# Kernel optimization log

Hardware: AMD Instinct MI355X
Metric: run time of the kernel (lower is better)

The kernel has to match this reference:

```python
import jax, jax.numpy as jnp
import numpy as np

B, S, DIN, DOUT = 4, 512, 4096, 10240


def setup_inputs() -> dict:
    key = jax.random.key(0)
    k1, k2, k3, k4 = jax.random.split(key, 4)
    # Activation in fp16, as the module casts input to self.dtype (fp16)
    input_tensor = jax.random.normal(k1, (B, S, DIN), dtype=jnp.float32).astype(jnp.float16)
    # weight emulates fp8 e4m3 storage; values here stand in for the dequant source
    weight = jax.random.normal(k2, (DOUT, DIN), dtype=jnp.float32) * 0.02
    # per-output-channel scale, stored fp32
    weight_scale = jax.random.uniform(k3, (DOUT, 1), dtype=jnp.float32, minval=0.5, maxval=1.5)
    bias = (jax.random.normal(k4, (DOUT,), dtype=jnp.float32) * 0.02).astype(jnp.float16)
    return {"input_tensor": input_tensor, "weight": weight, "weight_scale": weight_scale, "bias": bias}


def reference(input_tensor, weight, weight_scale, bias):
    # Dequantize: fp8 weight -> fp16, multiply by per-row scale (cast to fp16)
    w16 = weight.astype(jnp.float16) * weight_scale.astype(jnp.float16)  # [DOUT, DIN]
    # F.linear: x @ W^T + b, all in fp16
    out = jnp.einsum('bsi,oi->bso', input_tensor, w16) + bias  # [B, S, DOUT]
    return out
```

## Files before the change

### kernel.cpp

```cpp
#include <hip/hip_runtime.h>
#include <hip/hip_fp16.h>

typedef _Float16 half8 __attribute__((ext_vector_type(8)));
typedef float f32x4 __attribute__((ext_vector_type(4)));

constexpr int M = 2048;
constexpr int N = 10240;
constexpr int K = 4096;

__global__ __launch_bounds__(256)
void dequant_w_kernel(const float* __restrict__ W, const float* __restrict__ Wsc,
                      _Float16* __restrict__ Wh) {
    const long total = (long)N * K / 8;
    for (long i = (long)blockIdx.x * blockDim.x + threadIdx.x; i < total;
         i += (long)gridDim.x * blockDim.x) {
        const long base = i * 8;
        const int row = (int)(base >> 12);
        const _Float16 s = (_Float16)Wsc[row];
        const float4 w0 = ((const float4*)(W + base))[0];
        const float4 w1 = ((const float4*)(W + base))[1];
        half8 h;
        h[0] = (_Float16)w0.x * s; h[1] = (_Float16)w0.y * s;
        h[2] = (_Float16)w0.z * s; h[3] = (_Float16)w0.w * s;
        h[4] = (_Float16)w1.x * s; h[5] = (_Float16)w1.y * s;
        h[6] = (_Float16)w1.z * s; h[7] = (_Float16)w1.w * s;
        *(half8*)(Wh + base) = h;
    }
}

__global__ __launch_bounds__(256)
void convert_a_kernel(const float* __restrict__ A, _Float16* __restrict__ Ah) {
    const long total = (long)M * K / 8;
    for (long i = (long)blockIdx.x * blockDim.x + threadIdx.x; i < total;
         i += (long)gridDim.x * blockDim.x) {
        const long base = i * 8;
        const float4 a0 = ((const float4*)(A + base))[0];
        const float4 a1 = ((const float4*)(A + base))[1];
        half8 h;
        h[0] = (_Float16)a0.x; h[1] = (_Float16)a0.y;
        h[2] = (_Float16)a0.z; h[3] = (_Float16)a0.w;
        h[4] = (_Float16)a1.x; h[5] = (_Float16)a1.y;
        h[6] = (_Float16)a1.z; h[7] = (_Float16)a1.w;
        *(half8*)(Ah + base) = h;
    }
}

constexpr int BM = 128, BN = 320, BK = 64;
constexpr int AELE = BM * BK;
constexpr int BELE = BN * BK;
constexpr int NT = K / BK;

#define BAR()   asm volatile("s_barrier" ::: "memory")
#define LGKM0() asm volatile("s_waitcnt lgkmcnt(0)" ::: "memory")

__device__ __forceinline__ half8 lds_rd(const _Float16* base, int row, int eo) {
    const int ps = (eo >> 3) ^ (row & 7);
    return *(const half8*)(base + row * BK + ps * 8);
}

__global__ __launch_bounds__(512, 1)
void qgemm320_kernel(const _Float16* __restrict__ Ag,
                     const _Float16* __restrict__ Wg,
                     const float*    __restrict__ bias,
                     float*          __restrict__ C)
{
    __shared__ _Float16 AsF[2 * AELE];
    __shared__ _Float16 BsF[2 * BELE];

    const int orig = blockIdx.x;
    const int wgid = (orig & 7) * 64 + (orig >> 3);
    const int m0 = (wgid & 15) * BM;
    const int n0 = (wgid >> 4) * BN;

    const int tid  = threadIdx.x;
    const int lane = tid & 63;
    const int w    = tid >> 6;
    const int wm   = w >> 2;
    const int wn   = w & 3;
    const int fr   = lane & 15;
    const int fkE  = (lane >> 4) * 8;

    const int trow  = tid >> 3;
    const int swcol = (((tid & 7) ^ (trow & 7))) * 8;

    auto stage_a = [&](int b, int u, int kcol) {
        const _Float16* src = Ag + (size_t)(m0 + u * 64 + trow) * K + (kcol + swcol);
        __builtin_amdgcn_global_load_lds(
            (const __attribute__((address_space(1))) void*)src,
            (__attribute__((address_space(3))) void*)(AsF + b * AELE + u * 4096 + tid * 8),
            16, 0, 0);
    };
    auto stage_b = [&](int b, int u, int kcol) {
        const _Float16* src = Wg + (size_t)(n0 + u * 64 + trow) * K + (kcol + swcol);
        __builtin_amdgcn_global_load_lds(
            (const __attribute__((address_space(1))) void*)src,
            (__attribute__((address_space(3))) void*)(BsF + b * BELE + u * 4096 + tid * 8),
            16, 0, 0);
    };

    f32x4 acc[4][5];
#pragma unroll
    for (int i = 0; i < 4; ++i)
#pragma unroll
        for (int j = 0; j < 5; ++j)
            acc[i][j] = (f32x4){0.f, 0.f, 0.f, 0.f};

    stage_a(0, 0, 0); stage_a(0, 1, 0);
#pragma unroll
    for (int u = 0; u < 5; ++u) stage_b(0, u, 0);
    stage_a(1, 0, BK); stage_a(1, 1, BK);
#pragma unroll
    for (int u = 0; u < 5; ++u) stage_b(1, u, BK);
    asm volatile("s_waitcnt vmcnt(7)" ::: "memory");
    BAR();

#pragma unroll 1
    for (int t = 0; t < NT; ++t) {
        const int cur = t & 1;
        const _Float16* Ab = AsF + cur * AELE;
        const _Float16* Bb = BsF + cur * BELE;
        const bool pf2 = (t + 2 < NT);
        const int k2 = (t + 2) * BK;

        half8 af[4][2], bf[5][2];

#pragma unroll
        for (int rb = 0; rb < 4; ++rb)
#pragma unroll
            for (int kh = 0; kh < 2; ++kh)
                af[rb][kh] = lds_rd(Ab, wm * 64 + rb * 16 + fr, kh * 32 + fkE);
#pragma unroll
        for (int cb = 0; cb < 5; ++cb)
#pragma unroll
            for (int kh = 0; kh < 2; ++kh)
                bf[cb][kh] = lds_rd(Bb, wn * 80 + cb * 16 + fr, kh * 32 + fkE);

        __builtin_amdgcn_s_setprio(1);
#pragma unroll
        for (int rb = 0; rb < 4; ++rb)
#pragma unroll
            for (int cb = 0; cb < 3; ++cb)
#pragma unroll
                for (int kh = 0; kh < 2; ++kh)
                    acc[rb][cb] = __builtin_amdgcn_mfma_f32_16x16x32_f16(
                        af[rb][kh], bf[cb][kh], acc[rb][cb], 0, 0, 0);
        __builtin_amdgcn_s_setprio(0);

        LGKM0();
        BAR();

        if (pf2) {
            stage_a(cur, 0, k2); stage_a(cur, 1, k2);
#pragma unroll
            for (int u = 0; u < 5; ++u) stage_b(cur, u, k2);
        }
        __builtin_amdgcn_s_setprio(1);
#pragma unroll
        for (int rb = 0; rb < 4; ++rb)
#pragma unroll
            for (int cb = 3; cb < 5; ++cb)
#pragma unroll
                for (int kh = 0; kh < 2; ++kh)
                    acc[rb][cb] = __builtin_amdgcn_mfma_f32_16x16x32_f16(
                        af[rb][kh], bf[cb][kh], acc[rb][cb], 0, 0, 0);
        __builtin_amdgcn_s_setprio(0);

        if (pf2) asm volatile("s_waitcnt vmcnt(7)" ::: "memory");
        else     asm volatile("s_waitcnt vmcnt(0)" ::: "memory");
        BAR();
    }

    float bb[5];
#pragma unroll
    for (int j = 0; j < 5; ++j)
        bb[j] = bias[n0 + wn * 80 + j * 16 + fr];
#pragma unroll
    for (int i = 0; i < 4; ++i) {
        const int row = m0 + wm * 64 + i * 16 + (lane >> 4) * 4;
#pragma unroll
        for (int j = 0; j < 5; ++j) {
            const int col = n0 + wn * 80 + j * 16 + fr;
#pragma unroll
            for (int r = 0; r < 4; ++r)
                C[(size_t)(row + r) * N + col] =
                    (float)(_Float16)(acc[i][j][r] + bb[j]);
        }
    }
}

__global__ __launch_bounds__(256, 2)
void qlinear_fused_kernel(const float* __restrict__ A, const float* __restrict__ W,
                          const float* __restrict__ Wsc, const float* __restrict__ bias,
                          float* __restrict__ C)
{
    __shared__ _Float16 As[128][64];
    __shared__ _Float16 Bs[128][64];

    const int nwg  = (M / 128) * (N / 128);
    const int orig = blockIdx.x;
    const int wgid = (orig & 7) * (nwg >> 3) + (orig >> 3);
    const int brow = wgid & (M / 128 - 1);
    const int bcol = wgid / (M / 128);
    const int m0 = brow * 128;
    const int n0 = bcol * 128;

    const int t    = threadIdx.x;
    const int lane = t & 63;
    const int wave = t >> 6;
    const int wr = (wave >> 1) * 64;
    const int wc = (wave & 1) * 64;
    const int fr = lane & 15;
    const int fk = (lane >> 4) * 8;
    const int srow = t >> 3;
    const int scol = (t & 7) * 8;

    _Float16 hs[4];
#pragma unroll
    for (int p = 0; p < 4; ++p)
        hs[p] = (_Float16)Wsc[n0 + srow + p * 32];

    f32x4 acc[4][4];
#pragma unroll
    for (int i = 0; i < 4; ++i)
#pragma unroll
        for (int j = 0; j < 4; ++j)
            acc[i][j] = (f32x4){0.f, 0.f, 0.f, 0.f};

    for (int k0 = 0; k0 < K; k0 += 64) {
        __syncthreads();
#pragma unroll
        for (int c = 0; c < 4; ++c) {
            const int rl = c * 32 + srow;
            const float* asrc = A + (size_t)(m0 + rl) * K + (k0 + scol);
            const float4 a0 = ((const float4*)asrc)[0];
            const float4 a1 = ((const float4*)asrc)[1];
            half8 av;
            av[0] = (_Float16)a0.x; av[1] = (_Float16)a0.y;
            av[2] = (_Float16)a0.z; av[3] = (_Float16)a0.w;
            av[4] = (_Float16)a1.x; av[5] = (_Float16)a1.y;
            av[6] = (_Float16)a1.z; av[7] = (_Float16)a1.w;
            *(half8*)&As[rl][scol] = av;
        }
#pragma unroll
        for (int p = 0; p < 4; ++p) {
            const int nl = srow + p * 32;
            const float* wsrc = W + (size_t)(n0 + nl) * K + (k0 + scol);
            const float4 w0 = ((const float4*)wsrc)[0];
            const float4 w1 = ((const float4*)wsrc)[1];
            half8 hv;
            hv[0] = (_Float16)w0.x * hs[p]; hv[1] = (_Float16)w0.y * hs[p];
            hv[2] = (_Float16)w0.z * hs[p]; hv[3] = (_Float16)w0.w * hs[p];
            hv[4] = (_Float16)w1.x * hs[p]; hv[5] = (_Float16)w1.y * hs[p];
            hv[6] = (_Float16)w1.z * hs[p]; hv[7] = (_Float16)w1.w * hs[p];
            *(half8*)&Bs[nl][scol] = hv;
        }
        __syncthreads();
#pragma unroll
        for (int kk = 0; kk < 64; kk += 32) {
            half8 av[4], bv[4];
#pragma unroll
            for (int i = 0; i < 4; ++i)
                av[i] = *(const half8*)&As[wr + i * 16 + fr][kk + fk];
#pragma unroll
            for (int j = 0; j < 4; ++j)
                bv[j] = *(const half8*)&Bs[wc + j * 16 + fr][kk + fk];
#pragma unroll
            for (int i = 0; i < 4; ++i)
#pragma unroll
                for (int j = 0; j < 4; ++j)
                    acc[i][j] = __builtin_amdgcn_mfma_f32_16x16x32_f16(
                        av[i], bv[j], acc[i][j], 0, 0, 0);
        }
    }
#pragma unroll
    for (int i = 0; i < 4; ++i) {
        const int row = m0 + wr + i * 16 + (lane >> 4) * 4;
#pragma unroll
        for (int j = 0; j < 4; ++j) {
            const int col = n0 + wc + j * 16 + fr;
            const float bbf = bias[col];
#pragma unroll
            for (int r = 0; r < 4; ++r)
                C[(size_t)(row + r) * N + col] =
                    (float)(_Float16)(acc[i][j][r] + bbf);
        }
    }
}

extern "C" void kernel_launch(void* const* d_in, const int* in_sizes, int n_in,
                              void* d_out, int out_size, void* d_ws, size_t ws_size,
                              hipStream_t stream) {
    const float* A    = (const float*)d_in[0];
    const float* W    = (const float*)d_in[1];
    const float* Wsc  = (const float*)d_in[2];
    const float* bias = (const float*)d_in[3];
    float* C = (float*)d_out;

    const size_t a_bytes = (size_t)M * K * sizeof(_Float16);
    const size_t w_bytes = (size_t)N * K * sizeof(_Float16);

    if (ws_size >= a_bytes + w_bytes) {
        _Float16* Ah = (_Float16*)d_ws;
        _Float16* Wh = (_Float16*)((char*)d_ws + a_bytes);
        convert_a_kernel<<<dim3(1024), dim3(256), 0, stream>>>(A, Ah);
        dequant_w_kernel<<<dim3(2048), dim3(256), 0, stream>>>(W, Wsc, Wh);
        const int nwg = (M / BM) * (N / BN);
        qgemm320_kernel<<<dim3(nwg), dim3(512), 0, stream>>>(Ah, Wh, bias, C);
    } else {
        const int nwg = (M / 128) * (N / 128);
        qlinear_fused_kernel<<<dim3(nwg), dim3(256), 0, stream>>>(A, W, Wsc, bias, C);
    }
}
```

Baseline: 231.5 us.

## Stream B fragments directly from global into registers, keep only A in LDS

The GEMM kernel no longer stages the weight tile in shared memory. Each wave loads its B fragments straight from global memory into registers, prefetching the next K-step between MFMA groups, while A still goes through a double-buffered swizzled LDS tile filled with register loads and ds writes instead of global_load_lds. This shrinks LDS use and allows two workgroups per CU (launch bounds 512,2). In exchange, B reads are uncoalesced per-lane 16-byte loads with no reuse across the four waves that share columns, and each K-step now has two barriers.

Result: slower. 374.2 us (+61.7%).

```diff
diff --git a/kernel.cpp b/kernel.cpp
--- a/kernel.cpp
+++ b/kernel.cpp
@@ -47,7 +47,6 @@
 
 constexpr int BM = 128, BN = 320, BK = 64;
 constexpr int AELE = BM * BK;
-constexpr int BELE = BN * BK;
 constexpr int NT = K / BK;
 
 #define BAR()   asm volatile("s_barrier" ::: "memory")
@@ -58,14 +57,13 @@
     return *(const half8*)(base + row * BK + ps * 8);
 }
 
-__global__ __launch_bounds__(512, 1)
-void qgemm320_kernel(const _Float16* __restrict__ Ag,
-                     const _Float16* __restrict__ Wg,
-                     const float*    __restrict__ bias,
-                     float*          __restrict__ C)
+__global__ __launch_bounds__(512, 2)
+void qgemm_bstream_kernel(const _Float16* __restrict__ Ag,
+                          const _Float16* __restrict__ Wg,
+                          const float*    __restrict__ bias,
+                          float*          __restrict__ C)
 {
     __shared__ _Float16 AsF[2 * AELE];
-    __shared__ _Float16 BsF[2 * BELE];
 
     const int orig = blockIdx.x;
     const int wgid = (orig & 7) * 64 + (orig >> 3);
@@ -80,23 +78,14 @@
     const int fr   = lane & 15;
     const int fkE  = (lane >> 4) * 8;
 
-    const int trow  = tid >> 3;
-    const int swcol = (((tid & 7) ^ (trow & 7))) * 8;
-
-    auto stage_a = [&](int b, int u, int kcol) {
-        const _Float16* src = Ag + (size_t)(m0 + u * 64 + trow) * K + (kcol + swcol);
-        __builtin_amdgcn_global_load_lds(
-            (const __attribute__((address_space(1))) void*)src,
-            (__attribute__((address_space(3))) void*)(AsF + b * AELE + u * 4096 + tid * 8),
-            16, 0, 0);
-    };
-    auto stage_b = [&](int b, int u, int kcol) {
-        const _Float16* src = Wg + (size_t)(n0 + u * 64 + trow) * K + (kcol + swcol);
-        __builtin_amdgcn_global_load_lds(
-            (const __attribute__((address_space(1))) void*)src,
-            (__attribute__((address_space(3))) void*)(BsF + b * BELE + u * 4096 + tid * 8),
-            16, 0, 0);
-    };
+    const int arow   = tid >> 2;
+    const int aslot0 = (tid & 3) * 2;
+    const int acol   = aslot0 * 8;
+
+    const _Float16* bsrc[5];
+#pragma unroll
+    for (int cb = 0; cb < 5; ++cb)
+        bsrc[cb] = Wg + (size_t)(n0 + wn * 80 + cb * 16 + fr) * K + fkE;
 
     f32x4 acc[4][5];
 #pragma unroll
@@ -105,69 +94,68 @@
         for (int j = 0; j < 5; ++j)
             acc[i][j] = (f32x4){0.f, 0.f, 0.f, 0.f};
 
-    stage_a(0, 0, 0); stage_a(0, 1, 0);
-#pragma unroll
-    for (int u = 0; u < 5; ++u) stage_b(0, u, 0);
-    stage_a(1, 0, BK); stage_a(1, 1, BK);
-#pragma unroll
-    for (int u = 0; u < 5; ++u) stage_b(1, u, BK);
-    asm volatile("s_waitcnt vmcnt(7)" ::: "memory");
-    BAR();
+    const _Float16* a_src = Ag + (size_t)(m0 + arow) * K + acol;
+    half8 ar0 = *(const half8*)(a_src);
+    half8 ar1 = *(const half8*)(a_src + 8);
+    half8 bf[5][2];
+#pragma unroll
+    for (int cb = 0; cb < 5; ++cb)
+#pragma unroll
+        for (int kh = 0; kh < 2; ++kh)
+            bf[cb][kh] = *(const half8*)(bsrc[cb] + kh * 32);
+    {
+        _Float16* wdst = AsF + arow * BK;
+        *(half8*)(wdst + ((aslot0)     ^ (arow & 7)) * 8) = ar0;
+        *(half8*)(wdst + ((aslot0 + 1) ^ (arow & 7)) * 8) = ar1;
+    }
+    LGKM0(); BAR();
 
 #pragma unroll 1
     for (int t = 0; t < NT; ++t) {
-        const int cur = t & 1;
+        const int cur = t & 1, nxt = cur ^ 1;
         const _Float16* Ab = AsF + cur * AELE;
-        const _Float16* Bb = BsF + cur * BELE;
-        const bool pf2 = (t + 2 < NT);
-        const int k2 = (t + 2) * BK;
-
-        half8 af[4][2], bf[5][2];
-
+        const bool pf = (t + 1 < NT);
+        const int k1 = (t + 1) * BK;
+
+        half8 af[4][2];
 #pragma unroll
         for (int rb = 0; rb < 4; ++rb)
 #pragma unroll
             for (int kh = 0; kh < 2; ++kh)
                 af[rb][kh] = lds_rd(Ab, wm * 64 + rb * 16 + fr, kh * 32 + fkE);
-#pragma unroll
-        for (int cb = 0; cb < 5; ++cb)
-#pragma unroll
-            for (int kh = 0; kh < 2; ++kh)
-                bf[cb][kh] = lds_rd(Bb, wn * 80 + cb * 16 + fr, kh * 32 + fkE);
+
+        if (pf) {
+            const _Float16* s = Ag + (size_t)(m0 + arow) * K + k1 + acol;
+            ar0 = *(const half8*)(s);
+            ar1 = *(const half8*)(s + 8);
+        }
 
         __builtin_amdgcn_s_setprio(1);
 #pragma unroll
-        for (int rb = 0; rb < 4; ++rb)
-#pragma unroll
-            for (int cb = 0; cb < 3; ++cb)
+        for (int cb = 0; cb < 5; ++cb) {
+#pragma unroll
+            for (int rb = 0; rb < 4; ++rb)
 #pragma unroll
                 for (int kh = 0; kh < 2; ++kh)
                     acc[rb][cb] = __builtin_amdgcn_mfma_f32_16x16x32_f16(
                         af[rb][kh], bf[cb][kh], acc[rb][cb], 0, 0, 0);
+            if (pf) {
+#pragma unroll
+                for (int kh = 0; kh < 2; ++kh)
+                    bf[cb][kh] = *(const half8*)(bsrc[cb] + k1 + kh * 32);
+            }
+        }
         __builtin_amdgcn_s_setprio(0);
 
-        LGKM0();
-        BAR();
-
-        if (pf2) {
-            stage_a(cur, 0, k2); stage_a(cur, 1, k2);
-#pragma unroll
-            for (int u = 0; u < 5; ++u) stage_b(cur, u, k2);
-        }
-        __builtin_amdgcn_s_setprio(1);
-#pragma unroll
-        for (int rb = 0; rb < 4; ++rb)
-#pragma unroll
-            for (int cb = 3; cb < 5; ++cb)
-#pragma unroll
-                for (int kh = 0; kh < 2; ++kh)
-                    acc[rb][cb] = __builtin_amdgcn_mfma_f32_16x16x32_f16(
-                        af[rb][kh], bf[cb][kh], acc[rb][cb], 0, 0, 0);
-        __builtin_amdgcn_s_setprio(0);
-
-        if (pf2) asm volatile("s_waitcnt vmcnt(7)" ::: "memory");
-        else     asm volatile("s_waitcnt vmcnt(0)" ::: "memory");
-        BAR();
+        LGKM0(); BAR();
+
+        if (pf) {
+            _Float16* wdst = AsF + nxt * AELE + arow * BK;
+            *(half8*)(wdst + ((aslot0)     ^ (arow & 7)) * 8) = ar0;
+            *(half8*)(wdst + ((aslot0 + 1) ^ (arow & 7)) * 8) = ar1;
+        }
+
+        LGKM0(); BAR();
     }
 
     float bb[5];
@@ -305,7 +293,7 @@
         convert_a_kernel<<<dim3(1024), dim3(256), 0, stream>>>(A, Ah);
         dequant_w_kernel<<<dim3(2048), dim3(256), 0, stream>>>(W, Wsc, Wh);
         const int nwg = (M / BM) * (N / BN);
-        qgemm320_kernel<<<dim3(nwg), dim3(512), 0, stream>>>(Ah, Wh, bias, C);
+        qgemm_bstream_kernel<<<dim3(nwg), dim3(512), 0, stream>>>(Ah, Wh, bias, C);
     } else {
         const int nwg = (M / 128) * (N / 128);
         qlinear_fused_kernel<<<dim3(nwg), dim3(256), 0, stream>>>(A, W, Wsc, bias, C);
```
